# Kernel tuning notes

Hardware: AMD Instinct MI355X
Metric: run time of the kernel (lower is better)

The kernel has to match this reference:

```python
import jax, jax.numpy as jnp
import numpy as np

INPUT_LAYER_SIZE = 40960 * 2
LAYER1_SIZE = 512
LAYER2_SIZE = 32
LAYER3_SIZE = 32
BATCH = 4096


def setup_inputs() -> dict:
    key = jax.random.key(0)
    ks = jax.random.split(key, 10)
    # Sparse one-hot style features: mostly zeros with ~30 active entries per side.
    def sparse_features(k, n_active=30):
        kidx, = jax.random.split(k, 1)
        idx = jax.random.randint(kidx, (BATCH, n_active), 0, 40960)
        feats = jnp.zeros((BATCH, 40960), dtype=jnp.float32)
        return feats.at[jnp.arange(BATCH)[:, None], idx].set(1.0)
    w_features = sparse_features(ks[0])
    b_features = sparse_features(ks[1])
    s_in = 1.0 / np.sqrt(INPUT_LAYER_SIZE)
    s1 = 1.0 / np.sqrt(LAYER1_SIZE)
    s2 = 1.0 / np.sqrt(LAYER2_SIZE)
    s3 = 1.0 / np.sqrt(LAYER3_SIZE)
    return {
        "w_features": w_features,
        "b_features": b_features,
        "W_in": jax.random.uniform(ks[2], (LAYER1_SIZE, INPUT_LAYER_SIZE), jnp.float32, -s_in, s_in),
        "b_in": jax.random.uniform(ks[3], (LAYER1_SIZE,), jnp.float32, -s_in, s_in),
        "W1": jax.random.uniform(ks[4], (LAYER2_SIZE, LAYER1_SIZE), jnp.float32, -s1, s1),
        "b1": jax.random.uniform(ks[5], (LAYER2_SIZE,), jnp.float32, -s1, s1),
        "W2": jax.random.uniform(ks[6], (LAYER3_SIZE, LAYER2_SIZE), jnp.float32, -s2, s2),
        "b2": jax.random.uniform(ks[7], (LAYER3_SIZE,), jnp.float32, -s2, s2),
        "W3": jax.random.uniform(ks[8], (1, LAYER3_SIZE), jnp.float32, -s3, s3),
        "b3": jax.random.uniform(ks[9], (1,), jnp.float32, -s3, s3),
    }


def reference(w_features, b_features, W_in, b_in, W1, b1, W2, b2, W3, b3):
    # Concatenate both perspectives: [B, 81920]
    x = jnp.concatenate([w_features, b_features], axis=1)
    # Huge sparse-input accumulator layer (the kernel-headroom op)
    accum = x @ W_in.T + b_in                       # [B, 512]
    l1 = jnp.clip(accum, 0.0, 1.0)                  # clipped ReLU
    l2 = jnp.clip(l1 @ W1.T + b1, 0.0, 1.0)         # [B, 32]
    l3 = jnp.clip(l2 @ W2.T + b2, 0.0, 1.0)         # [B, 32]
    return l3 @ W3.T + b3                           # [B, 1]
```

## Files before the change

### kernel.cpp

```cpp
#include <hip/hip_runtime.h>
#include <hip/hip_bf16.h>

#define IN_PER_SIDE   40960
#define IN_TOTAL      81920
#define L1            512
#define L2            32
#define L3_           32
#define BATCH         4096
#define MAXIDX        128

typedef float        v4f __attribute__((ext_vector_type(4)));
typedef float        v8f __attribute__((ext_vector_type(8)));
typedef _Float16     v4h __attribute__((ext_vector_type(4)));
typedef _Float16     v8h __attribute__((ext_vector_type(8)));
typedef unsigned int v4u __attribute__((ext_vector_type(4)));

#define WT_BYTES ((size_t)IN_TOTAL * L1 * sizeof(_Float16))
#define CNT_OFF  WT_BYTES
#define IDX_OFF  (WT_BYTES + 16384)
#define WS_NEED  (IDX_OFF + (size_t)BATCH * MAXIDX * 4)

__global__ __launch_bounds__(256) void zero_cnt(int* __restrict__ cnt)
{
    cnt[blockIdx.x * 256 + threadIdx.x] = 0;
}

__global__ __launch_bounds__(256) void prep(
    const float* __restrict__ W, _Float16* __restrict__ WTh,
    const float* __restrict__ wf, const float* __restrict__ bfeat,
    int* __restrict__ cnt, int* __restrict__ idxg)
{
    __shared__ float tile[64][65];
    const int jt = (blockIdx.x % 1280) * 64;
    const int ot = (blockIdx.x / 1280) * 64;

    {
        const int tx = threadIdx.x & 15;
        const int ty = threadIdx.x >> 4;
#pragma unroll
        for (int k = 0; k < 4; ++k) {
            const int o = ty + 16 * k;
            const v4f* p = (const v4f*)&W[(size_t)(ot + o) * IN_TOTAL + jt + 4 * tx];
            v4f v = __builtin_nontemporal_load(p);
            tile[4 * tx + 0][o] = v.x;
            tile[4 * tx + 1][o] = v.y;
            tile[4 * tx + 2][o] = v.z;
            tile[4 * tx + 3][o] = v.w;
        }
    }
    __syncthreads();
    {
        const int tx = threadIdx.x & 7;
        const int ty = threadIdx.x >> 3;
#pragma unroll
        for (int k = 0; k < 2; ++k) {
            const int j = ty + 32 * k;
            v8f v;
#pragma unroll
            for (int c = 0; c < 8; ++c) v[c] = tile[j][8 * tx + c];
            v8h h = __builtin_convertvector(v, v8h);
            *(v8h*)&WTh[(size_t)(jt + j) * L1 + ot + 8 * tx] = h;
        }
    }

    const v4u* wv = (const v4u*)wf;
    const v4u* bv = (const v4u*)bfeat;
    const size_t base = (size_t)blockIdx.x * 4096 + threadIdx.x;
#pragma unroll 4
    for (int u = 0; u < 16; ++u) {
        const size_t i = base + (size_t)u * 256;
        const v4u a = __builtin_nontemporal_load(wv + i);
        const v4u c = __builtin_nontemporal_load(bv + i);
        if (a.x | a.y | a.z | a.w) {
            const int row = (int)(i / 10240);
            const int fb  = (int)(i % 10240) * 4;
            int* lst = idxg + (size_t)row * MAXIDX;
            if (a.x) { int p = atomicAdd(&cnt[row], 1); if (p < MAXIDX) lst[p] = fb + 0; }
            if (a.y) { int p = atomicAdd(&cnt[row], 1); if (p < MAXIDX) lst[p] = fb + 1; }
            if (a.z) { int p = atomicAdd(&cnt[row], 1); if (p < MAXIDX) lst[p] = fb + 2; }
            if (a.w) { int p = atomicAdd(&cnt[row], 1); if (p < MAXIDX) lst[p] = fb + 3; }
        }
        if (c.x | c.y | c.z | c.w) {
            const int row = (int)(i / 10240);
            const int fb  = IN_PER_SIDE + (int)(i % 10240) * 4;
            int* lst = idxg + (size_t)row * MAXIDX;
            if (c.x) { int p = atomicAdd(&cnt[row], 1); if (p < MAXIDX) lst[p] = fb + 0; }
            if (c.y) { int p = atomicAdd(&cnt[row], 1); if (p < MAXIDX) lst[p] = fb + 1; }
            if (c.z) { int p = atomicAdd(&cnt[row], 1); if (p < MAXIDX) lst[p] = fb + 2; }
            if (c.w) { int p = atomicAdd(&cnt[row], 1); if (p < MAXIDX) lst[p] = fb + 3; }
        }
    }
}

__global__ __launch_bounds__(512) void nnue_fused(
    const _Float16* __restrict__ WTh,
    const int* __restrict__ cnt, const int* __restrict__ idxg,
    const float* __restrict__ b_in,
    const float* __restrict__ W1, const float* __restrict__ b1,
    const float* __restrict__ W2, const float* __restrict__ b2,
    const float* __restrict__ W3, const float* __restrict__ b3,
    float* __restrict__ out)
{
    const int b = blockIdx.x;
    const int t = threadIdx.x;

    __shared__ int   sidx[MAXIDX];
    __shared__ float accs[8 * 64 * 9];
    __shared__ float l1s[L1];
    __shared__ float l2acc[L2];
    __shared__ float l2s[L2];
    __shared__ float l3s[L3_];

    const int n = min(cnt[b], MAXIDX);
    if (t < MAXIDX) {
        const int g = idxg[(size_t)b * MAXIDX + t];
        sidx[t] = (t < n) ? g : 0;
    }
    __syncthreads();

    const int w = t >> 6;
    const int l = t & 63;
    const v8h* WTH8 = (const v8h*)WTh;

    v8f acc0 = {0, 0, 0, 0, 0, 0, 0, 0};
    v8f acc1 = {0, 0, 0, 0, 0, 0, 0, 0};
    const int J     = (n + 7) >> 3;
    const int Jeven = (J + 1) & ~1;

    {
        const int f0 = w, f1 = w + 8;
        v8h h0 = WTH8[(size_t)sidx[f0 < n ? f0 : 0] * 64 + l];
        float s0 = (f0 < n) ? 1.0f : 0.0f;
        v8h h1 = WTH8[(size_t)sidx[f1 < n ? f1 : 0] * 64 + l];
        float s1 = (f1 < n) ? 1.0f : 0.0f;
        for (int j = 2; j < Jeven; j += 2) {
            const int g0 = w + 8 * j, g1 = g0 + 8;
            v8h p0 = WTH8[(size_t)sidx[g0 < n ? g0 : 0] * 64 + l];
            const float u0 = (g0 < n) ? 1.0f : 0.0f;
            v8h p1 = WTH8[(size_t)sidx[g1 < n ? g1 : 0] * 64 + l];
            const float u1 = (g1 < n) ? 1.0f : 0.0f;
            acc0 += s0 * __builtin_convertvector(h0, v8f);
            acc1 += s1 * __builtin_convertvector(h1, v8f);
            h0 = p0; s0 = u0; h1 = p1; s1 = u1;
        }
        acc0 += s0 * __builtin_convertvector(h0, v8f);
        acc1 += s1 * __builtin_convertvector(h1, v8f);
    }
    acc0 += acc1;

    {
        float* dst = &accs[(w * 64 + l) * 9];
#pragma unroll
        for (int i = 0; i < 8; ++i) dst[i] = acc0[i];
    }
    __syncthreads();

    {
        const int ll = t >> 3, c = t & 7;
        float s = 0.0f;
#pragma unroll
        for (int ww = 0; ww < 8; ++ww) s += accs[(ww * 64 + ll) * 9 + c];
        l1s[t] = fminf(fmaxf(s + b_in[t], 0.0f), 1.0f);
    }
    __syncthreads();

    {
        const int kk = t >> 4;
        const int gg = t & 15;
        const float* wp = W1 + (size_t)kk * L1;
        float p = 0.0f;
        for (int o = gg; o < L1; o += 16) p += wp[o] * l1s[o];
#pragma unroll
        for (int off = 8; off > 0; off >>= 1) p += __shfl_down(p, off, 16);
        if (gg == 0) l2acc[kk] = p;
    }
    __syncthreads();
    if (t < L2) l2s[t] = fminf(fmaxf(l2acc[t] + b1[t], 0.0f), 1.0f);
    __syncthreads();

    if (t < L3_) {
        const float* wp = W2 + (size_t)t * L2;
        float p = b2[t];
#pragma unroll
        for (int q = 0; q < L2; ++q) p += wp[q] * l2s[q];
        l3s[t] = fminf(fmaxf(p, 0.0f), 1.0f);
    }
    __syncthreads();

    if (t == 0) {
        float p = b3[0];
#pragma unroll
        for (int q = 0; q < L3_; ++q) p += W3[q] * l3s[q];
        out[b] = p;
    }
}

__global__ __launch_bounds__(512) void nnue_fallback(
    const float* __restrict__ wf, const float* __restrict__ bfeat,
    const float* __restrict__ W_in, const float* __restrict__ b_in,
    const float* __restrict__ W1, const float* __restrict__ b1,
    const float* __restrict__ W2, const float* __restrict__ b2,
    const float* __restrict__ W3, const float* __restrict__ b3,
    float* __restrict__ out)
{
    const int b = blockIdx.x;
    const int t = threadIdx.x;
    __shared__ int   idxs[MAXIDX];
    __shared__ int   scnt;
    __shared__ float l1s[L1];
    __shared__ float l2acc[L2];
    __shared__ float l2s[L2];
    __shared__ float l3s[L3_];

    if (t == 0) scnt = 0;
    __syncthreads();
    const v4f* wrow = (const v4f*)(wf    + (size_t)b * IN_PER_SIDE);
    const v4f* brow = (const v4f*)(bfeat + (size_t)b * IN_PER_SIDE);
    for (int i = t; i < IN_PER_SIDE / 4; i += 512) {
        v4f v = wrow[i];
        if (v.x != 0.0f) idxs[atomicAdd(&scnt, 1)] = 4 * i + 0;
        if (v.y != 0.0f) idxs[atomicAdd(&scnt, 1)] = 4 * i + 1;
        if (v.z != 0.0f) idxs[atomicAdd(&scnt, 1)] = 4 * i + 2;
        if (v.w != 0.0f) idxs[atomicAdd(&scnt, 1)] = 4 * i + 3;
        v4f u = brow[i];
        if (u.x != 0.0f) idxs[atomicAdd(&scnt, 1)] = IN_PER_SIDE + 4 * i + 0;
        if (u.y != 0.0f) idxs[atomicAdd(&scnt, 1)] = IN_PER_SIDE + 4 * i + 1;
        if (u.z != 0.0f) idxs[atomicAdd(&scnt, 1)] = IN_PER_SIDE + 4 * i + 2;
        if (u.w != 0.0f) idxs[atomicAdd(&scnt, 1)] = IN_PER_SIDE + 4 * i + 3;
    }
    __syncthreads();
    const int n = scnt;
    float a0 = 0.0f;
    const float* row = W_in + (size_t)t * IN_TOTAL;
    for (int i = 0; i < n; ++i) a0 += row[idxs[i]];
    l1s[t] = fminf(fmaxf(b_in[t] + a0, 0.0f), 1.0f);
    __syncthreads();
    {
        const int k = t >> 4, g = t & 15;
        const float* wp = W1 + (size_t)k * L1;
        float p = 0.0f;
        for (int o = g; o < L1; o += 16) p += wp[o] * l1s[o];
#pragma unroll
        for (int off = 8; off > 0; off >>= 1) p += __shfl_down(p, off, 16);
        if (g == 0) l2acc[k] = p;
    }
    __syncthreads();
    if (t < L2) l2s[t] = fminf(fmaxf(l2acc[t] + b1[t], 0.0f), 1.0f);
    __syncthreads();
    if (t < L3_) {
        const float* wp = W2 + (size_t)t * L2;
        float p = b2[t];
#pragma unroll
        for (int q = 0; q < L2; ++q) p += wp[q] * l2s[q];
        l3s[t] = fminf(fmaxf(p, 0.0f), 1.0f);
    }
    __syncthreads();
    if (t == 0) {
        float p = b3[0];
#pragma unroll
        for (int q = 0; q < L3_; ++q) p += W3[q] * l3s[q];
        out[b] = p;
    }
}

extern "C" void kernel_launch(void* const* d_in, const int* in_sizes, int n_in,
                              void* d_out, int out_size, void* d_ws, size_t ws_size,
                              hipStream_t stream) {
    const float* wf   = (const float*)d_in[0];
    const float* bfeat= (const float*)d_in[1];
    const float* W_in = (const float*)d_in[2];
    const float* b_in = (const float*)d_in[3];
    const float* W1   = (const float*)d_in[4];
    const float* b1   = (const float*)d_in[5];
    const float* W2   = (const float*)d_in[6];
    const float* b2   = (const float*)d_in[7];
    const float* W3   = (const float*)d_in[8];
    const float* b3   = (const float*)d_in[9];
    float* out = (float*)d_out;

    if (ws_size >= WS_NEED) {
        char* ws = (char*)d_ws;
        _Float16* WTh = (_Float16*)ws;
        int* cnt  = (int*)(ws + CNT_OFF);
        int* idxg = (int*)(ws + IDX_OFF);
        zero_cnt<<<BATCH / 256, 256, 0, stream>>>(cnt);
        prep<<<10240, 256, 0, stream>>>(W_in, WTh, wf, bfeat, cnt, idxg);
        nnue_fused<<<BATCH, 512, 0, stream>>>(
            WTh, cnt, idxg, b_in, W1, b1, W2, b2, W3, b3, out);
    } else {
        nnue_fallback<<<BATCH, 512, 0, stream>>>(
            wf, bfeat, W_in, b_in, W1, b1, W2, b2, W3, b3, out);
    }
}
```

Measured before the change: 1.400 ms.

## Split prep into separate transpose and per-row feature scan kernels

Splits the combined weight transpose plus sparse-index extraction kernel into two kernels. The transpose uses a 2D grid. The feature scan gives each (row, side) pair its own block, which collects indices in shared memory with LDS atomics and then issues a single global atomic per block, replacing the per-element global atomics. This adds a kernel launch and loses any overlap between the transpose and scan work inside one kernel.

```diff
diff --git a/kernel.cpp b/kernel.cpp
--- a/kernel.cpp
+++ b/kernel.cpp
@@ -25,14 +25,12 @@
     cnt[blockIdx.x * 256 + threadIdx.x] = 0;
 }
 
-__global__ __launch_bounds__(256) void prep(
-    const float* __restrict__ W, _Float16* __restrict__ WTh,
-    const float* __restrict__ wf, const float* __restrict__ bfeat,
-    int* __restrict__ cnt, int* __restrict__ idxg)
+__global__ __launch_bounds__(256) void transpose_win(
+    const float* __restrict__ W, _Float16* __restrict__ WTh)
 {
     __shared__ float tile[64][65];
-    const int jt = (blockIdx.x % 1280) * 64;
-    const int ot = (blockIdx.x / 1280) * 64;
+    const int jt = blockIdx.x * 64;
+    const int ot = blockIdx.y * 64;
 
     {
         const int tx = threadIdx.x & 15;
@@ -62,37 +60,45 @@
             *(v8h*)&WTh[(size_t)(jt + j) * L1 + ot + 8 * tx] = h;
         }
     }
-
-    const v4u* wv = (const v4u*)wf;
-    const v4u* bv = (const v4u*)bfeat;
-    const size_t base = (size_t)blockIdx.x * 4096 + threadIdx.x;
-#pragma unroll 4
-    for (int u = 0; u < 16; ++u) {
-        const size_t i = base + (size_t)u * 256;
-        const v4u a = __builtin_nontemporal_load(wv + i);
-        const v4u c = __builtin_nontemporal_load(bv + i);
+}
+
+__global__ __launch_bounds__(256) void scan_rows(
+    const float* __restrict__ wf, const float* __restrict__ bfeat,
+    int* __restrict__ cnt, int* __restrict__ idxg)
+{
+    const int r = blockIdx.x >> 1;
+    const int s = blockIdx.x & 1;
+    const int t = threadIdx.x;
+
+    __shared__ int lidx[MAXIDX];
+    __shared__ int lcnt;
+    __shared__ int lbase;
+    if (t == 0) lcnt = 0;
+    __syncthreads();
+
+    const float* src = s ? bfeat : wf;
+    const int    off = s ? IN_PER_SIDE : 0;
+    const v4u* row = (const v4u*)(src + (size_t)r * IN_PER_SIDE);
+
+    for (int i = t; i < IN_PER_SIDE / 4; i += 256) {
+        const v4u a = __builtin_nontemporal_load(row + i);
         if (a.x | a.y | a.z | a.w) {
-            const int row = (int)(i / 10240);
-            const int fb  = (int)(i % 10240) * 4;
-            int* lst = idxg + (size_t)row * MAXIDX;
-            if (a.x) { int p = atomicAdd(&cnt[row], 1); if (p < MAXIDX) lst[p] = fb + 0; }
-            if (a.y) { int p = atomicAdd(&cnt[row], 1); if (p < MAXIDX) lst[p] = fb + 1; }
-            if (a.z) { int p = atomicAdd(&cnt[row], 1); if (p < MAXIDX) lst[p] = fb + 2; }
-            if (a.w) { int p = atomicAdd(&cnt[row], 1); if (p < MAXIDX) lst[p] = fb + 3; }
-        }
-        if (c.x | c.y | c.z | c.w) {
-            const int row = (int)(i / 10240);
-            const int fb  = IN_PER_SIDE + (int)(i % 10240) * 4;
-            int* lst = idxg + (size_t)row * MAXIDX;
-            if (c.x) { int p = atomicAdd(&cnt[row], 1); if (p < MAXIDX) lst[p] = fb + 0; }
-            if (c.y) { int p = atomicAdd(&cnt[row], 1); if (p < MAXIDX) lst[p] = fb + 1; }
-            if (c.z) { int p = atomicAdd(&cnt[row], 1); if (p < MAXIDX) lst[p] = fb + 2; }
-            if (c.w) { int p = atomicAdd(&cnt[row], 1); if (p < MAXIDX) lst[p] = fb + 3; }
-        }
-    }
-}
-
-__global__ __launch_bounds__(512) void nnue_fused(
+            if (a.x) { int p = atomicAdd(&lcnt, 1); if (p < MAXIDX) lidx[p] = off + 4 * i + 0; }
+            if (a.y) { int p = atomicAdd(&lcnt, 1); if (p < MAXIDX) lidx[p] = off + 4 * i + 1; }
+            if (a.z) { int p = atomicAdd(&lcnt, 1); if (p < MAXIDX) lidx[p] = off + 4 * i + 2; }
+            if (a.w) { int p = atomicAdd(&lcnt, 1); if (p < MAXIDX) lidx[p] = off + 4 * i + 3; }
+        }
+    }
+    __syncthreads();
+    const int nb = min(lcnt, MAXIDX);
+    if (t == 0) lbase = atomicAdd(&cnt[r], nb);
+    __syncthreads();
+    const int b0 = lbase;
+    if (t < nb && b0 + t < MAXIDX)
+        idxg[(size_t)r * MAXIDX + b0 + t] = lidx[t];
+}
+
+__global__ __launch_bounds__(512) void nnue_gather(
     const _Float16* __restrict__ WTh,
     const int* __restrict__ cnt, const int* __restrict__ idxg,
     const float* __restrict__ b_in,
@@ -283,9 +289,14 @@
         _Float16* WTh = (_Float16*)ws;
         int* cnt  = (int*)(ws + CNT_OFF);
         int* idxg = (int*)(ws + IDX_OFF);
+
         zero_cnt<<<BATCH / 256, 256, 0, stream>>>(cnt);
-        prep<<<10240, 256, 0, stream>>>(W_in, WTh, wf, bfeat, cnt, idxg);
-        nnue_fused<<<BATCH, 512, 0, stream>>>(
+        {
+            dim3 grid(IN_TOTAL / 64, L1 / 64);
+            transpose_win<<<grid, 256, 0, stream>>>(W_in, WTh);
+        }
+        scan_rows<<<2 * BATCH, 256, 0, stream>>>(wf, bfeat, cnt, idxg);
+        nnue_gather<<<BATCH, 512, 0, stream>>>(
             WTh, cnt, idxg, b_in, W1, b1, W2, b2, W3, b3, out);
     } else {
         nnue_fallback<<<BATCH, 512, 0, stream>>>(
```

Result: faster. 1.373 ms (-2.0%).
